# Optimization experiments

Measured on AMD Instinct MI355X. Metric: run time of the kernel, lower is better.

The kernel has to match this reference:

```python
import jax, jax.numpy as jnp
import numpy as np

N_STEPS = 256          # ray-marching samples per ray
DENSITY_SCALE = 10.0   # sigma scale (extinction coefficient multiplier)
EPS = 1e-8


def _trilerp(grid, x, y, z):
    """Trilinear interpolation. grid: [D,H,W]; x,y,z: voxel coords ([...])."""
    D, H, W = grid.shape
    x0 = jnp.clip(jnp.floor(x), 0, W - 2).astype(jnp.int32)
    y0 = jnp.clip(jnp.floor(y), 0, H - 2).astype(jnp.int32)
    z0 = jnp.clip(jnp.floor(z), 0, D - 2).astype(jnp.int32)
    fx = jnp.clip(x - x0, 0.0, 1.0)
    fy = jnp.clip(y - y0, 0.0, 1.0)
    fz = jnp.clip(z - z0, 0.0, 1.0)
    x1, y1, z1 = x0 + 1, y0 + 1, z0 + 1
    c000 = grid[z0, y0, x0]; c001 = grid[z0, y0, x1]
    c010 = grid[z0, y1, x0]; c011 = grid[z0, y1, x1]
    c100 = grid[z1, y0, x0]; c101 = grid[z1, y0, x1]
    c110 = grid[z1, y1, x0]; c111 = grid[z1, y1, x1]
    c00 = c000 * (1 - fx) + c001 * fx
    c01 = c010 * (1 - fx) + c011 * fx
    c10 = c100 * (1 - fx) + c101 * fx
    c11 = c110 * (1 - fx) + c111 * fx
    c0 = c00 * (1 - fy) + c01 * fy
    c1 = c10 * (1 - fy) + c11 * fy
    return c0 * (1 - fz) + c1 * fz


def _transmittance(rays, grid):
    """rays: [N,6] (origin, direction); grid: [D,H,W] clamped densities in [0,1].
    Marches through the [-1,1]^3 box and returns per-ray transmittance [N]."""
    D, H, W = grid.shape
    o = rays[:, 0:3]                                  # [N,3]
    d = rays[:, 3:6]
    d = d / (jnp.linalg.norm(d, axis=-1, keepdims=True) + EPS)
    # ray-box intersection with the unit box [-1,1]^3 (safe reciprocal)
    inv_d = 1.0 / jnp.where(jnp.abs(d) < EPS, jnp.sign(d) * EPS + EPS, d)
    t_a = (-1.0 - o) * inv_d
    t_b = (1.0 - o) * inv_d
    tmin = jnp.max(jnp.minimum(t_a, t_b), axis=-1)    # [N]
    tmax = jnp.min(jnp.maximum(t_a, t_b), axis=-1)
    tmin = jnp.maximum(tmin, 0.0)
    valid = tmax > tmin
    seg = jnp.where(valid, tmax - tmin, 0.0)          # traversed length
    # midpoint sample positions along each ray: [N, S, 3]
    frac = (jnp.arange(N_STEPS, dtype=grid.dtype) + 0.5) / N_STEPS
    ts = tmin[:, None] + seg[:, None] * frac[None, :]          # [N,S]
    pos = o[:, None, :] + ts[:, :, None] * d[:, None, :]        # [N,S,3]
    # map [-1,1] -> voxel coordinates
    gx = (pos[..., 0] + 1.0) * 0.5 * (W - 1)
    gy = (pos[..., 1] + 1.0) * 0.5 * (H - 1)
    gz = (pos[..., 2] + 1.0) * 0.5 * (D - 1)
    sigma = _trilerp(grid, gx, gy, gz)                 # [N,S]
    dt = seg / N_STEPS                                 # [N]
    tau = DENSITY_SCALE * jnp.sum(sigma, axis=-1) * dt
    return jnp.where(valid, jnp.exp(-tau), 1.0)


def setup_inputs() -> dict:
    key = jax.random.key(0)
    k_rays, k_grid = jax.random.split(key)
    rays = jax.random.normal(k_rays, (65536, 6), dtype=jnp.float32)
    grid = jax.random.uniform(k_grid, (256, 256, 256), dtype=jnp.float32)
    return {"rays": rays, "Grid": grid}


def reference(rays, Grid):
    # TrainableCloud.forward: renderer(rays, clamp(Grid, 0, 1))
    return _transmittance(rays, jnp.clip(Grid, 0.0, 1.0))
```

## Files before the change

kernel.cpp:

```cpp
#include <hip/hip_runtime.h>
#include <hip/hip_fp16.h>
#include <math.h>
#include <stdint.h>

#define N_STEPS 256
#define DENSITY_SCALE 10.0f
#define REF_EPS 1e-8f

typedef uint32_t u32_a2 __attribute__((aligned(2)));
typedef uint2 uint2_a4 __attribute__((aligned(4)));

__device__ __forceinline__ float clip01(float v) {
    return fminf(fmaxf(v, 0.0f), 1.0f);
}

__device__ __forceinline__ float safe_inv(float d) {
    float denom = d;
    if (fabsf(d) < REF_EPS) {
        float s = (d > 0.0f) ? 1.0f : ((d < 0.0f) ? -1.0f : 0.0f);
        denom = s * REF_EPS + REF_EPS;
    }
    return 1.0f / denom;
}

__device__ __forceinline__ uint32_t q255(float v) {
    return (uint32_t)__float2int_rn(clip01(v) * 255.0f);
}

__global__ __launch_bounds__(256) void repack_quad_kernel(
    const float* __restrict__ g, uint32_t* __restrict__ quad)
{
    int t = blockIdx.x * blockDim.x + threadIdx.x;
    int x4 = (t & 63) << 2;
    int zy = t >> 6;
    int z = zy >> 8;
    int y = zy & 255;
    int yp = (y == 255) ? y : y + 1;
    int zp = (z == 255) ? z : z + 1;
    float4 a = *(const float4*)(g + ((z  << 16) + (y  << 8) + x4));
    float4 b = *(const float4*)(g + ((z  << 16) + (yp << 8) + x4));
    float4 c = *(const float4*)(g + ((zp << 16) + (y  << 8) + x4));
    float4 d = *(const float4*)(g + ((zp << 16) + (yp << 8) + x4));
    uint4 o;
    o.x = q255(a.x) | (q255(b.x) << 8) | (q255(c.x) << 16) | (q255(d.x) << 24);
    o.y = q255(a.y) | (q255(b.y) << 8) | (q255(c.y) << 16) | (q255(d.y) << 24);
    o.z = q255(a.z) | (q255(b.z) << 8) | (q255(c.z) << 16) | (q255(d.z) << 24);
    o.w = q255(a.w) | (q255(b.w) << 8) | (q255(c.w) << 16) | (q255(d.w) << 24);
    *(uint4*)(quad + ((zy << 8) + x4)) = o;
}

__global__ __launch_bounds__(256, 8) void march_all_kernel(
    const float* __restrict__ rays, const uint32_t* __restrict__ quad,
    float* __restrict__ out, int n_rays)
{
    int gid = blockIdx.x * blockDim.x + threadIdx.x;
    int sub = gid & 15;
    int stride = (gridDim.x * blockDim.x) >> 4;

    for (int ray = gid >> 4; ray < n_rays; ray += stride) {
        const float* r = rays + ray * 6;
        float ox = r[0], oy = r[1], oz = r[2];
        float dx = r[3], dy = r[4], dz = r[5];
        float nrm = sqrtf(dx*dx + dy*dy + dz*dz) + REF_EPS;
        float inv_n = 1.0f / nrm;
        dx *= inv_n; dy *= inv_n; dz *= inv_n;
        float ixv = safe_inv(dx), iyv = safe_inv(dy), izv = safe_inv(dz);
        float tax = (-1.0f - ox) * ixv, tbx = (1.0f - ox) * ixv;
        float tay = (-1.0f - oy) * iyv, tby = (1.0f - oy) * iyv;
        float taz = (-1.0f - oz) * izv, tbz = (1.0f - oz) * izv;
        float tmin = fmaxf(fmaxf(fminf(tax, tbx), fminf(tay, tby)), fminf(taz, tbz));
        float tmax = fminf(fminf(fmaxf(tax, tbx), fmaxf(tay, tby)), fmaxf(taz, tbz));
        tmin = fmaxf(tmin, 0.0f);
        if (!(tmax > tmin)) {
            if (sub == 0) out[ray] = 1.0f;
            continue;
        }
        float seg = tmax - tmin;

        float s   = seg * (1.0f / (float)N_STEPS);
        float t0  = fmaf(0.5f, s, tmin);
        float dxs = dx * 127.5f, dys = dy * 127.5f, dzs = dz * 127.5f;
        float gsx = dxs * s, gsy = dys * s, gsz = dzs * s;
        float gx0 = fmaf(t0, dxs, fmaf(ox, 127.5f, 127.5f));
        float gy0 = fmaf(t0, dys, fmaf(oy, 127.5f, 127.5f));
        float gz0 = fmaf(t0, dzs, fmaf(oz, 127.5f, 127.5f));

        float sum = 0.0f;
        #pragma unroll 8
        for (int i = sub; i < N_STEPS; i += 16) {
            float fi = (float)i;
            float gx = fmaf(fi, gsx, gx0);
            float gy = fmaf(fi, gsy, gy0);
            float gz = fmaf(fi, gsz, gz0);

            float fx0 = floorf(gx), fy0 = floorf(gy), fz0 = floorf(gz);
            int x0 = (int)fminf(fmaxf(fx0, 0.0f), 254.0f);
            int y0 = (int)fminf(fmaxf(fy0, 0.0f), 254.0f);
            int z0 = (int)fminf(fmaxf(fz0, 0.0f), 254.0f);
            float fx = fminf(fmaxf(gx - (float)x0, 0.0f), 1.0f);
            float fy = fminf(fmaxf(gy - (float)y0, 0.0f), 1.0f);
            float fz = fminf(fmaxf(gz - (float)z0, 0.0f), 1.0f);

            int vidx = (z0 << 16) + (y0 << 8) + x0;
            uint2 v = *(const uint2_a4*)(quad + vidx);
            float c000 = (float)( v.x        & 0xffu);
            float c010 = (float)((v.x >>  8) & 0xffu);
            float c100 = (float)((v.x >> 16) & 0xffu);
            float c110 = (float)( v.x >> 24        );
            float c001 = (float)( v.y        & 0xffu);
            float c011 = (float)((v.y >>  8) & 0xffu);
            float c101 = (float)((v.y >> 16) & 0xffu);
            float c111 = (float)( v.y >> 24        );

            float omfx = 1.0f - fx;
            float c00 = c000 * omfx + c001 * fx;
            float c01 = c010 * omfx + c011 * fx;
            float c10 = c100 * omfx + c101 * fx;
            float c11 = c110 * omfx + c111 * fx;
            float omfy = 1.0f - fy;
            float cc0 = c00 * omfy + c01 * fy;
            float cc1 = c10 * omfy + c11 * fy;
            sum += cc0 * (1.0f - fz) + cc1 * fz;
        }

        sum += __shfl_xor(sum, 1);
        sum += __shfl_xor(sum, 2);
        sum += __shfl_xor(sum, 4);
        sum += __shfl_xor(sum, 8);

        if (sub == 0) {
            float dt = seg * (1.0f / (float)N_STEPS);
            float tau = (DENSITY_SCALE / 255.0f) * sum * dt;
            out[ray] = expf(-tau);
        }
    }
}

__global__ __launch_bounds__(256) void repack_kernel(
    const float* __restrict__ g, __half* __restrict__ gh, int n)
{
    int i = (blockIdx.x * blockDim.x + threadIdx.x) * 4;
    if (i >= n) return;
    float4 v = *(const float4*)(g + i);
    __half2* dst = (__half2*)(gh + i);
    dst[0] = __floats2half2_rn(clip01(v.x), clip01(v.y));
    dst[1] = __floats2half2_rn(clip01(v.z), clip01(v.w));
}

__global__ __launch_bounds__(256) void transmittance_h_kernel(
    const float* __restrict__ rays, const __half* __restrict__ gh,
    float* __restrict__ out, int n_rays)
{
    int gid = blockIdx.x * blockDim.x + threadIdx.x;
    int ray = gid >> 3;
    int sub = gid & 7;
    if (ray >= n_rays) return;

    const float* r = rays + ray * 6;
    float ox = r[0], oy = r[1], oz = r[2];
    float dx = r[3], dy = r[4], dz = r[5];
    float nrm = sqrtf(dx*dx + dy*dy + dz*dz) + REF_EPS;
    float inv_n = 1.0f / nrm;
    dx *= inv_n; dy *= inv_n; dz *= inv_n;
    float ixv = safe_inv(dx), iyv = safe_inv(dy), izv = safe_inv(dz);
    float tax = (-1.0f - ox) * ixv, tbx = (1.0f - ox) * ixv;
    float tay = (-1.0f - oy) * iyv, tby = (1.0f - oy) * iyv;
    float taz = (-1.0f - oz) * izv, tbz = (1.0f - oz) * izv;
    float tmin = fmaxf(fmaxf(fminf(tax, tbx), fminf(tay, tby)), fminf(taz, tbz));
    float tmax = fminf(fminf(fmaxf(tax, tbx), fmaxf(tay, tby)), fmaxf(taz, tbz));
    tmin = fmaxf(tmin, 0.0f);
    bool valid = tmax > tmin;
    float seg = valid ? (tmax - tmin) : 0.0f;
    float sum = 0.0f;

    if (valid) {
        #pragma unroll 4
        for (int i = sub; i < N_STEPS; i += 8) {
            float frac = ((float)i + 0.5f) * (1.0f / (float)N_STEPS);
            float t = fmaf(seg, frac, tmin);
            float px = fmaf(t, dx, ox);
            float py = fmaf(t, dy, oy);
            float pz = fmaf(t, dz, oz);
            float gx = (px + 1.0f) * (0.5f * 255.0f);
            float gy = (py + 1.0f) * (0.5f * 255.0f);
            float gz = (pz + 1.0f) * (0.5f * 255.0f);
            float fx0 = floorf(gx), fy0 = floorf(gy), fz0 = floorf(gz);
            int x0 = (int)fminf(fmaxf(fx0, 0.0f), 254.0f);
            int y0 = (int)fminf(fmaxf(fy0, 0.0f), 254.0f);
            int z0 = (int)fminf(fmaxf(fz0, 0.0f), 254.0f);
            float fx = fminf(fmaxf(gx - (float)x0, 0.0f), 1.0f);
            float fy = fminf(fmaxf(gy - (float)y0, 0.0f), 1.0f);
            float fz = fminf(fmaxf(gz - (float)z0, 0.0f), 1.0f);
            const __half* p0 = gh + ((z0 << 16) + (y0 << 8) + x0);
            u32_a2 a00 = *(const u32_a2*)(const void*)(p0);
            u32_a2 a01 = *(const u32_a2*)(const void*)(p0 + 256);
            u32_a2 a10 = *(const u32_a2*)(const void*)(p0 + 65536);
            u32_a2 a11 = *(const u32_a2*)(const void*)(p0 + 65536 + 256);
            float2 f00 = __half22float2(*(__half2*)&a00);
            float2 f01 = __half22float2(*(__half2*)&a01);
            float2 f10 = __half22float2(*(__half2*)&a10);
            float2 f11 = __half22float2(*(__half2*)&a11);
            float omfx = 1.0f - fx;
            float c00 = f00.x * omfx + f00.y * fx;
            float c01 = f01.x * omfx + f01.y * fx;
            float c10 = f10.x * omfx + f10.y * fx;
            float c11 = f11.x * omfx + f11.y * fx;
            float omfy = 1.0f - fy;
            float cc0 = c00 * omfy + c01 * fy;
            float cc1 = c10 * omfy + c11 * fy;
            sum += cc0 * (1.0f - fz) + cc1 * fz;
        }
    }

    sum += __shfl_xor(sum, 1);
    sum += __shfl_xor(sum, 2);
    sum += __shfl_xor(sum, 4);

    if (sub == 0) {
        float result = 1.0f;
        if (valid) {
            float dt = seg * (1.0f / (float)N_STEPS);
            float tau = DENSITY_SCALE * sum * dt;
            result = expf(-tau);
        }
        out[ray] = result;
    }
}

__global__ __launch_bounds__(256) void transmittance_kernel(
    const float* __restrict__ rays, const float* __restrict__ grid,
    float* __restrict__ out, int n_rays)
{
    int gid = blockIdx.x * blockDim.x + threadIdx.x;
    int ray = gid >> 2;
    int sub = gid & 3;
    if (ray >= n_rays) return;
    const float* r = rays + ray * 6;
    float ox = r[0], oy = r[1], oz = r[2];
    float dx = r[3], dy = r[4], dz = r[5];
    float nrm = sqrtf(dx*dx + dy*dy + dz*dz) + REF_EPS;
    float inv_n = 1.0f / nrm;
    dx *= inv_n; dy *= inv_n; dz *= inv_n;
    float ixv = safe_inv(dx), iyv = safe_inv(dy), izv = safe_inv(dz);
    float tax = (-1.0f - ox) * ixv, tbx = (1.0f - ox) * ixv;
    float tay = (-1.0f - oy) * iyv, tby = (1.0f - oy) * iyv;
    float taz = (-1.0f - oz) * izv, tbz = (1.0f - oz) * izv;
    float tmin = fmaxf(fmaxf(fminf(tax, tbx), fminf(tay, tby)), fminf(taz, tbz));
    float tmax = fminf(fminf(fmaxf(tax, tbx), fmaxf(tay, tby)), fmaxf(taz, tbz));
    tmin = fmaxf(tmin, 0.0f);
    bool valid = tmax > tmin;
    float result = 1.0f;
    float seg = valid ? (tmax - tmin) : 0.0f;
    float sum = 0.0f;
    if (valid) {
        #pragma unroll 4
        for (int i = sub; i < N_STEPS; i += 4) {
            float frac = ((float)i + 0.5f) * (1.0f / (float)N_STEPS);
            float t = fmaf(seg, frac, tmin);
            float px = fmaf(t, dx, ox);
            float py = fmaf(t, dy, oy);
            float pz = fmaf(t, dz, oz);
            float gx = (px + 1.0f) * (0.5f * 255.0f);
            float gy = (py + 1.0f) * (0.5f * 255.0f);
            float gz = (pz + 1.0f) * (0.5f * 255.0f);
            float fx0 = floorf(gx), fy0 = floorf(gy), fz0 = floorf(gz);
            int x0 = (int)fminf(fmaxf(fx0, 0.0f), 254.0f);
            int y0 = (int)fminf(fmaxf(fy0, 0.0f), 254.0f);
            int z0 = (int)fminf(fmaxf(fz0, 0.0f), 254.0f);
            float fx = fminf(fmaxf(gx - (float)x0, 0.0f), 1.0f);
            float fy = fminf(fmaxf(gy - (float)y0, 0.0f), 1.0f);
            float fz = fminf(fmaxf(gz - (float)z0, 0.0f), 1.0f);
            const float* p0 = grid + ((z0 << 16) + (y0 << 8) + x0);
            const float* p1 = p0 + 65536;
            float c000 = p0[0],   c001 = p0[1];
            float c010 = p0[256], c011 = p0[257];
            float c100 = p1[0],   c101 = p1[1];
            float c110 = p1[256], c111 = p1[257];
            float omfx = 1.0f - fx;
            float c00 = c000 * omfx + c001 * fx;
            float c01 = c010 * omfx + c011 * fx;
            float c10 = c100 * omfx + c101 * fx;
            float c11 = c110 * omfx + c111 * fx;
            float omfy = 1.0f - fy;
            float cc0 = c00 * omfy + c01 * fy;
            float cc1 = c10 * omfy + c11 * fy;
            sum += cc0 * (1.0f - fz) + cc1 * fz;
        }
    }
    sum += __shfl_xor(sum, 1);
    sum += __shfl_xor(sum, 2);
    if (valid) {
        float dt = seg * (1.0f / (float)N_STEPS);
        float tau = DENSITY_SCALE * sum * dt;
        result = expf(-tau);
    }
    if (sub == 0) out[ray] = result;
}

extern "C" void kernel_launch(void* const* d_in, const int* in_sizes, int n_in,
                              void* d_out, int out_size, void* d_ws, size_t ws_size,
                              hipStream_t stream) {
    const float* rays = (const float*)d_in[0];
    const float* grid = (const float*)d_in[1];
    float* out = (float*)d_out;
    int n_rays = in_sizes[0] / 6;
    int n_grid = in_sizes[1];

    const size_t QUAD_BYTES = (size_t)n_grid * 4;
    const size_t need_half  = (size_t)n_grid * 2;

    if (ws_size >= QUAD_BYTES) {
        uint32_t* quad = (uint32_t*)d_ws;
        int rp_threads = n_grid / 4;
        repack_quad_kernel<<<(rp_threads + 255) / 256, 256, 0, stream>>>(grid, quad);
        march_all_kernel<<<4096, 256, 0, stream>>>(rays, quad, out, n_rays);
    } else if (ws_size >= need_half) {
        __half* gh = (__half*)d_ws;
        int rp_threads = n_grid / 4;
        repack_kernel<<<(rp_threads + 255) / 256, 256, 0, stream>>>(grid, gh, n_grid);
        int total_threads = n_rays * 8;
        transmittance_h_kernel<<<(total_threads + 255) / 256, 256, 0, stream>>>(
            rays, gh, out, n_rays);
    } else {
        int total_threads = n_rays * 4;
        transmittance_kernel<<<(total_threads + 255) / 256, 256, 0, stream>>>(
            rays, grid, out, n_rays);
    }
}
```

Before: 161.7 us.

## Repack quantized grid into 4x2x2 bricks for better gather locality

Replaces the row-major packed-quad layout with a brick layout where each 4x2x2 block of voxels (each holding a 2x2 yz corner quad) occupies 64 contiguous bytes. The repack kernel now loads a 3x3 set of rows per brick, and the march kernel computes brick-relative addresses and issues two 32-bit loads instead of one unaligned 64-bit load. The aim is to improve cache-line locality for rays that move in y and z, at the cost of extra address arithmetic and a second load instruction per sample.

Result: faster. 151.0 us (-6.6%).

```diff
diff --git a/kernel.cpp b/kernel.cpp
--- a/kernel.cpp
+++ b/kernel.cpp
@@ -8,7 +8,6 @@
 #define REF_EPS 1e-8f
 
 typedef uint32_t u32_a2 __attribute__((aligned(2)));
-typedef uint2 uint2_a4 __attribute__((aligned(4)));
 
 __device__ __forceinline__ float clip01(float v) {
     return fminf(fmaxf(v, 0.0f), 1.0f);
@@ -27,26 +26,50 @@
     return (uint32_t)__float2int_rn(clip01(v) * 255.0f);
 }
 
-__global__ __launch_bounds__(256) void repack_quad_kernel(
+__global__ __launch_bounds__(256) void repack_brick_kernel(
     const float* __restrict__ g, uint32_t* __restrict__ quad)
 {
     int t = blockIdx.x * blockDim.x + threadIdx.x;
-    int x4 = (t & 63) << 2;
-    int zy = t >> 6;
-    int z = zy >> 8;
-    int y = zy & 255;
-    int yp = (y == 255) ? y : y + 1;
-    int zp = (z == 255) ? z : z + 1;
-    float4 a = *(const float4*)(g + ((z  << 16) + (y  << 8) + x4));
-    float4 b = *(const float4*)(g + ((z  << 16) + (yp << 8) + x4));
-    float4 c = *(const float4*)(g + ((zp << 16) + (y  << 8) + x4));
-    float4 d = *(const float4*)(g + ((zp << 16) + (yp << 8) + x4));
-    uint4 o;
-    o.x = q255(a.x) | (q255(b.x) << 8) | (q255(c.x) << 16) | (q255(d.x) << 24);
-    o.y = q255(a.y) | (q255(b.y) << 8) | (q255(c.y) << 16) | (q255(d.y) << 24);
-    o.z = q255(a.z) | (q255(b.z) << 8) | (q255(c.z) << 16) | (q255(d.z) << 24);
-    o.w = q255(a.w) | (q255(b.w) << 8) | (q255(c.w) << 16) | (q255(d.w) << 24);
-    *(uint4*)(quad + ((zy << 8) + x4)) = o;
+    int bx = t & 63;
+    int byz = t >> 6;
+    int by = byz & 127;
+    int bz = byz >> 7;
+    int x4 = bx << 2;
+    int y0 = by << 1;
+    int z0 = bz << 1;
+
+    uint32_t qr[3][3][4];
+    #pragma unroll
+    for (int dz = 0; dz < 3; ++dz) {
+        int z = z0 + dz; if (z > 255) z = 255;
+        #pragma unroll
+        for (int dy = 0; dy < 3; ++dy) {
+            int y = y0 + dy; if (y > 255) y = 255;
+            float4 r = *(const float4*)(g + ((z << 16) + (y << 8) + x4));
+            qr[dz][dy][0] = q255(r.x);
+            qr[dz][dy][1] = q255(r.y);
+            qr[dz][dy][2] = q255(r.z);
+            qr[dz][dy][3] = q255(r.w);
+        }
+    }
+
+    uint32_t* dst = quad + ((size_t)t << 4);
+    #pragma unroll
+    for (int lz = 0; lz < 2; ++lz) {
+        #pragma unroll
+        for (int ly = 0; ly < 2; ++ly) {
+            uint4 o;
+            uint32_t* po = (uint32_t*)&o;
+            #pragma unroll
+            for (int lx = 0; lx < 4; ++lx) {
+                po[lx] = qr[lz][ly][lx]
+                       | (qr[lz][ly + 1][lx] << 8)
+                       | (qr[lz + 1][ly][lx] << 16)
+                       | (qr[lz + 1][ly + 1][lx] << 24);
+            }
+            *(uint4*)(dst + ((ly << 2) + (lz << 3))) = o;
+        }
+    }
 }
 
 __global__ __launch_bounds__(256, 8) void march_all_kernel(
@@ -101,16 +124,21 @@
             float fy = fminf(fmaxf(gy - (float)y0, 0.0f), 1.0f);
             float fz = fminf(fmaxf(gz - (float)z0, 0.0f), 1.0f);
 
-            int vidx = (z0 << 16) + (y0 << 8) + x0;
-            uint2 v = *(const uint2_a4*)(quad + vidx);
-            float c000 = (float)( v.x        & 0xffu);
-            float c010 = (float)((v.x >>  8) & 0xffu);
-            float c100 = (float)((v.x >> 16) & 0xffu);
-            float c110 = (float)( v.x >> 24        );
-            float c001 = (float)( v.y        & 0xffu);
-            float c011 = (float)((v.y >>  8) & 0xffu);
-            float c101 = (float)((v.y >> 16) & 0xffu);
-            float c111 = (float)( v.y >> 24        );
+            int base = ((((z0 >> 1) << 13) + ((y0 >> 1) << 6)) << 4)
+                     + ((y0 & 1) << 2) + ((z0 & 1) << 3);
+            int x1 = x0 + 1;
+            int a0 = base + ((x0 >> 2) << 4) + (x0 & 3);
+            int a1 = base + ((x1 >> 2) << 4) + (x1 & 3);
+            uint32_t w0 = quad[a0];
+            uint32_t w1 = quad[a1];
+            float c000 = (float)( w0        & 0xffu);
+            float c010 = (float)((w0 >>  8) & 0xffu);
+            float c100 = (float)((w0 >> 16) & 0xffu);
+            float c110 = (float)( w0 >> 24        );
+            float c001 = (float)( w1        & 0xffu);
+            float c011 = (float)((w1 >>  8) & 0xffu);
+            float c101 = (float)((w1 >> 16) & 0xffu);
+            float c111 = (float)( w1 >> 24        );
 
             float omfx = 1.0f - fx;
             float c00 = c000 * omfx + c001 * fx;
@@ -311,8 +339,8 @@
 
     if (ws_size >= QUAD_BYTES) {
         uint32_t* quad = (uint32_t*)d_ws;
-        int rp_threads = n_grid / 4;
-        repack_quad_kernel<<<(rp_threads + 255) / 256, 256, 0, stream>>>(grid, quad);
+        int n_bricks = n_grid / 16;
+        repack_brick_kernel<<<n_bricks / 256, 256, 0, stream>>>(grid, quad);
         march_all_kernel<<<4096, 256, 0, stream>>>(rays, quad, out, n_rays);
     } else if (ws_size >= need_half) {
         __half* gh = (__half*)d_ws;
```
